# Performance work log

Measured on AMD Instinct MI355X. Metric: run time of the kernel, lower is better.

The kernel has to match this reference:

```python
import jax, jax.numpy as jnp
import numpy as np

NSIDE = 128
NPIX = 12 * NSIDE * NSIDE          # HEALPix pixel count, nested ordering
WIN = 16                           # window = 4x4 nested child block (w=1)
SHIFT = WIN // 2
EPS = 1e-5


def _ln(x, g, b):
    mu = x.mean(-1, keepdims=True)
    var = ((x - mu) ** 2).mean(-1, keepdims=True)
    return (x - mu) * jax.lax.rsqrt(var + EPS) * g + b


def _window_attn(x, wq, bq, wp, bp, n_heads):
    B, N, C = x.shape
    D = C // n_heads
    nw = N // WIN
    qkv = (x @ wq + bq).reshape(B, nw, WIN, 3, n_heads, D)
    q, k, v = jnp.moveaxis(qkv, 3, 0)
    q = jnp.swapaxes(q, 2, 3)
    k = jnp.swapaxes(k, 2, 3)
    v = jnp.swapaxes(v, 2, 3)
    scores = jnp.einsum('bwhqd,bwhkd->bwhqk', q, k) * (D ** -0.5)
    attn = jax.nn.softmax(scores, axis=-1)
    out = jnp.einsum('bwhqk,bwhkd->bwhqd', attn, v)
    out = jnp.swapaxes(out, 2, 3).reshape(B, N, C)
    return out @ wp + bp


def _transformer_block(x, p, shift, n_heads):
    if shift:
        x = jnp.roll(x, -SHIFT, axis=1)          # cyclic shift along nested index
    x = x + _window_attn(_ln(x, p['ln1_g'], p['ln1_b']),
                         p['w_qkv'], p['b_qkv'], p['w_proj'], p['b_proj'], n_heads)
    h = _ln(x, p['ln2_g'], p['ln2_b'])
    x = x + jax.nn.gelu(h @ p['w_mlp1'] + p['b_mlp1'], approximate=False) @ p['w_mlp2'] + p['b_mlp2']
    if shift:
        x = jnp.roll(x, SHIFT, axis=1)
    return x


def _forward(x, w_ff1, b_ff1, ln1_g, ln1_b, w_qkv, b_qkv, w_proj, b_proj,
             ln2_g, ln2_b, w_mlp1, b_mlp1, w_mlp2, b_mlp2, w_ff2, b_ff2,
             n_heads=4):
    residual = x
    h = jax.nn.gelu(x @ w_ff1 + b_ff1, approximate=False)
    for i, shift in enumerate((False, True)):
        p = dict(ln1_g=ln1_g[i], ln1_b=ln1_b[i], w_qkv=w_qkv[i], b_qkv=b_qkv[i],
                 w_proj=w_proj[i], b_proj=b_proj[i], ln2_g=ln2_g[i], ln2_b=ln2_b[i],
                 w_mlp1=w_mlp1[i], b_mlp1=b_mlp1[i], w_mlp2=w_mlp2[i], b_mlp2=b_mlp2[i])
        h = _transformer_block(h, p, shift, n_heads)
    return residual + h @ w_ff2 + b_ff2


def setup_inputs() -> dict:
    key = jax.random.key(0)
    ks = jax.random.split(key, 8)
    F, C, M = 64, 128, 512  # node_feat_dim, node_hidden_dim, mlp hidden
    s = 0.02
    return {
        'x': jax.random.normal(ks[0], (1, NPIX, F), jnp.float32),
        'w_ff1': jax.random.normal(ks[1], (F, C), jnp.float32) * s,
        'b_ff1': jnp.zeros((C,), jnp.float32),
        'ln1_g': jnp.ones((2, C), jnp.float32),
        'ln1_b': jnp.zeros((2, C), jnp.float32),
        'w_qkv': jax.random.normal(ks[2], (2, C, 3 * C), jnp.float32) * s,
        'b_qkv': jnp.zeros((2, 3 * C), jnp.float32),
        'w_proj': jax.random.normal(ks[3], (2, C, C), jnp.float32) * s,
        'b_proj': jnp.zeros((2, C), jnp.float32),
        'ln2_g': jnp.ones((2, C), jnp.float32),
        'ln2_b': jnp.zeros((2, C), jnp.float32),
        'w_mlp1': jax.random.normal(ks[4], (2, C, M), jnp.float32) * s,
        'b_mlp1': jnp.zeros((2, M), jnp.float32),
        'w_mlp2': jax.random.normal(ks[5], (2, M, C), jnp.float32) * s,
        'b_mlp2': jnp.zeros((2, C), jnp.float32),
        'w_ff2': jax.random.normal(ks[6], (C, F), jnp.float32) * s,
        'b_ff2': jnp.zeros((F,), jnp.float32),
    }


def reference(x, w_ff1, b_ff1, ln1_g, ln1_b, w_qkv, b_qkv, w_proj, b_proj,
              ln2_g, ln2_b, w_mlp1, b_mlp1, w_mlp2, b_mlp2, w_ff2, b_ff2):
    return _forward(x, w_ff1, b_ff1, ln1_g, ln1_b, w_qkv, b_qkv, w_proj, b_proj,
                    ln2_g, ln2_b, w_mlp1, b_mlp1, w_mlp2, b_mlp2, w_ff2, b_ff2)
```

## Files before the change

kernel.cpp:

```cpp
#include <hip/hip_runtime.h>
#include <hip/hip_bf16.h>
#include <math.h>

#define NPIX 196608
#define SCALE_Q 0.17677669529663687f

typedef __attribute__((ext_vector_type(4))) float f32x4;
typedef __attribute__((ext_vector_type(8))) short short8;
typedef __attribute__((ext_vector_type(4))) short short4v;
typedef __hip_bfloat16 bf16;

__device__ __forceinline__ float gelu_f(float x) {
    float yy = 1.5957691216057308f * (x + 0.044715f * x * x * x);
    float e = __expf(yy);
    return x - x * __builtin_amdgcn_rcpf(e + 1.0f);
}
__device__ __forceinline__ float gelu_fast(float x) {
    float e = __expf(-1.702f * x);
    return x * __builtin_amdgcn_rcpf(1.0f + e);
}

__device__ __forceinline__ short bfbits(float f) {
    bf16 h = __float2bfloat16(f);
    return *reinterpret_cast<short*>(&h);
}

__device__ __forceinline__ short8 ldsA(const bf16* buf, int row, int el) {
    return *reinterpret_cast<const short8*>(buf + row * 128 + (el ^ ((row & 7) << 3)));
}
__device__ __forceinline__ short8 ldsA64(const bf16* buf, int row, int el) {
    return *reinterpret_cast<const short8*>(buf + row * 64 + (el ^ ((row & 7) << 3)));
}
__device__ __forceinline__ short8 gld8(const bf16* p) {
    return *reinterpret_cast<const short8*>(p);
}

__device__ __forceinline__ void bar_lds() {
    asm volatile("s_waitcnt lgkmcnt(0)" ::: "memory");
    __builtin_amdgcn_s_barrier();
}

__global__ __launch_bounds__(256) void k_convert(
    const float* __restrict__ wff1, const float* __restrict__ wqkv,
    const float* __restrict__ wproj, const float* __restrict__ wmlp1,
    const float* __restrict__ wmlp2, const float* __restrict__ wff2,
    bf16* __restrict__ dst)
{
    int gid = blockIdx.x * 256 + threadIdx.x;
    if (gid < 8192) {
        int n = gid >> 6, k = gid & 63;
        dst[gid] = __float2bfloat16(wff1[k * 128 + n]);
    } else if (gid < 106496) {
        int r = gid - 8192; int l = r / 49152; r -= l * 49152;
        int n = r >> 7, k = r & 127;
        dst[gid] = __float2bfloat16(wqkv[l * 49152 + k * 384 + n]);
    } else if (gid < 139264) {
        int r = gid - 106496; int l = r / 16384; r -= l * 16384;
        int n = r >> 7, k = r & 127;
        dst[gid] = __float2bfloat16(wproj[l * 16384 + k * 128 + n]);
    } else if (gid < 270336) {
        int r = gid - 139264; int l = r >> 16; r &= 65535;
        int n = r >> 7, k = r & 127;
        dst[gid] = __float2bfloat16(wmlp1[l * 65536 + k * 512 + n]);
    } else if (gid < 401408) {
        int r = gid - 270336; int l = r >> 16; r &= 65535;
        int n = r >> 9, k = r & 511;
        dst[gid] = __float2bfloat16(wmlp2[l * 65536 + k * 128 + n]);
    } else if (gid < 409600) {
        int r = gid - 401408;
        int n = r >> 7, k = r & 127;
        dst[gid] = __float2bfloat16(wff2[k * 64 + n]);
    }
}

template <int OFFSET, int MODE>
__global__ __launch_bounds__(256, 3) void k_block(
    const float* __restrict__ x, float* __restrict__ h,
    const bf16* __restrict__ wf1t, const float* __restrict__ bf1,
    const float* __restrict__ g1, const float* __restrict__ be1,
    const bf16* __restrict__ wqt, const float* __restrict__ bq,
    const bf16* __restrict__ wpt, const float* __restrict__ bp,
    const float* __restrict__ g2, const float* __restrict__ be2,
    const bf16* __restrict__ w1t, const float* __restrict__ b1,
    const bf16* __restrict__ w2t, const float* __restrict__ b2,
    const bf16* __restrict__ wf2t, const float* __restrict__ bf2,
    float* __restrict__ out)
{
    __shared__ __align__(16) bf16 bufA[8192];
    __shared__ __align__(16) bf16 bufB[8192];
    __shared__ __align__(16) bf16 bufC[4096];
    const int tid = threadIdx.x, base = blockIdx.x * 64;
    const int wid = tid >> 6, lrow = tid & 15, lgrp = (tid >> 4) & 3;
    const int cb0 = wid * 32;
    const int hc  = wid * 32;

    f32x4 hraw[2][4];

    if (MODE == 0) {
        short8 wf1[2][2];
#pragma unroll
        for (int nt = 0; nt < 2; ++nt)
#pragma unroll
            for (int kk = 0; kk < 2; ++kk)
                wf1[nt][kk] = gld8(wf1t + (size_t)(cb0 + nt * 16 + lrow) * 64 + kk * 32 + lgrp * 8);
        {
            int row = tid >> 2, q = tid & 3;
#pragma unroll
            for (int s = 0; s < 2; ++s) {
                int gg = q + s * 4;
                const float4* src = reinterpret_cast<const float4*>(x + (size_t)(base + row) * 64 + gg * 8);
                float4 v0 = src[0], v1 = src[1];
                short8 w;
                w[0] = bfbits(v0.x); w[1] = bfbits(v0.y); w[2] = bfbits(v0.z); w[3] = bfbits(v0.w);
                w[4] = bfbits(v1.x); w[5] = bfbits(v1.y); w[6] = bfbits(v1.z); w[7] = bfbits(v1.w);
                *reinterpret_cast<short8*>(&bufC[row * 64 + ((gg * 8) ^ ((row & 7) << 3))]) = w;
            }
        }
        bar_lds();
        short8 xb1[4][2];
#pragma unroll
        for (int tt = 0; tt < 4; ++tt)
#pragma unroll
            for (int kk = 0; kk < 2; ++kk)
                xb1[tt][kk] = ldsA64(bufC, tt * 16 + lrow, kk * 32 + lgrp * 8);
#pragma unroll
        for (int nt = 0; nt < 2; ++nt) {
            float4 bv = *reinterpret_cast<const float4*>(bf1 + cb0 + nt * 16 + lgrp * 4);
#pragma unroll
            for (int tt = 0; tt < 4; ++tt) {
                f32x4 d = {0.f, 0.f, 0.f, 0.f};
#pragma unroll
                for (int kk = 0; kk < 2; ++kk)
                    d = __builtin_amdgcn_mfma_f32_16x16x32_bf16(wf1[nt][kk], xb1[tt][kk], d, 0, 0, 0);
                f32x4 r;
                r[0] = gelu_f(d[0] + bv.x); r[1] = gelu_f(d[1] + bv.y);
                r[2] = gelu_f(d[2] + bv.z); r[3] = gelu_f(d[3] + bv.w);
                hraw[nt][tt] = r;
            }
        }
    } else {
#pragma unroll
        for (int nt = 0; nt < 2; ++nt)
#pragma unroll
            for (int tt = 0; tt < 4; ++tt) {
                int tok = base + OFFSET + tt * 16 + lrow; if (tok >= NPIX) tok -= NPIX;
                float4 hv = *reinterpret_cast<const float4*>(h + (size_t)tok * 128 + cb0 + nt * 16 + lgrp * 4);
                f32x4 r; r[0] = hv.x; r[1] = hv.y; r[2] = hv.z; r[3] = hv.w;
                hraw[nt][tt] = r;
            }
    }

    float2* ws1 = reinterpret_cast<float2*>(bufB);
#pragma unroll
    for (int tt = 0; tt < 4; ++tt) {
        float s = 0.f, q = 0.f;
#pragma unroll
        for (int nt = 0; nt < 2; ++nt)
#pragma unroll
            for (int i = 0; i < 4; ++i) { float v = hraw[nt][tt][i]; s += v; q += v * v; }
        s += __shfl_xor(s, 16, 64); s += __shfl_xor(s, 32, 64);
        q += __shfl_xor(q, 16, 64); q += __shfl_xor(q, 32, 64);
        if (lgrp == 0) { float2 t2; t2.x = s; t2.y = q; ws1[wid * 64 + tt * 16 + lrow] = t2; }
    }
    bar_lds();
    {
        float mu[4], rstd[4];
#pragma unroll
        for (int tt = 0; tt < 4; ++tt) {
            float s = 0.f, q = 0.f;
#pragma unroll
            for (int w = 0; w < 4; ++w) {
                float2 t2 = ws1[w * 64 + tt * 16 + lrow];
                s += t2.x; q += t2.y;
            }
            float m = s * (1.f / 128.f);
            mu[tt] = m;
            rstd[tt] = rsqrtf(q * (1.f / 128.f) - m * m + 1e-5f);
        }
        float4 gv[2], bev[2];
#pragma unroll
        for (int nt = 0; nt < 2; ++nt) {
            gv[nt]  = *reinterpret_cast<const float4*>(g1 + cb0 + nt * 16 + lgrp * 4);
            bev[nt] = *reinterpret_cast<const float4*>(be1 + cb0 + nt * 16 + lgrp * 4);
        }
#pragma unroll
        for (int nt = 0; nt < 2; ++nt)
#pragma unroll
            for (int tt = 0; tt < 4; ++tt) {
                short4v pk;
                pk[0] = bfbits((hraw[nt][tt][0] - mu[tt]) * rstd[tt] * gv[nt].x + bev[nt].x);
                pk[1] = bfbits((hraw[nt][tt][1] - mu[tt]) * rstd[tt] * gv[nt].y + bev[nt].y);
                pk[2] = bfbits((hraw[nt][tt][2] - mu[tt]) * rstd[tt] * gv[nt].z + bev[nt].z);
                pk[3] = bfbits((hraw[nt][tt][3] - mu[tt]) * rstd[tt] * gv[nt].w + bev[nt].w);
                int row = tt * 16 + lrow;
                int c = cb0 + nt * 16 + lgrp * 4;
                *reinterpret_cast<short4v*>(&bufA[row * 128 + (c ^ ((row & 7) << 3))]) = pk;
            }
    }
    short8 wfp[2][4];
#pragma unroll
    for (int nt = 0; nt < 2; ++nt)
#pragma unroll
        for (int kk = 0; kk < 4; ++kk)
            wfp[nt][kk] = gld8(wpt + (size_t)(cb0 + nt * 16 + lrow) * 128 + kk * 32 + lgrp * 8);
    bar_lds();

    short8 xb[4][4];
#pragma unroll
    for (int tt = 0; tt < 4; ++tt)
#pragma unroll
        for (int kk = 0; kk < 4; ++kk)
            xb[tt][kk] = ldsA(bufA, tt * 16 + lrow, kk * 32 + lgrp * 8);
    bar_lds();

#pragma unroll
    for (int qt = 0; qt < 2; ++qt) {
        const int cb = hc + qt * 16;
        float4 bqv = *reinterpret_cast<const float4*>(bq + cb + lgrp * 4);
        short8 wf[4];
#pragma unroll
        for (int kk = 0; kk < 4; ++kk)
            wf[kk] = gld8(wqt + (size_t)(cb + lrow) * 128 + kk * 32 + lgrp * 8);
#pragma unroll
        for (int tt = 0; tt < 4; ++tt) {
            f32x4 d = {0.f, 0.f, 0.f, 0.f};
#pragma unroll
            for (int kk = 0; kk < 4; ++kk)
                d = __builtin_amdgcn_mfma_f32_16x16x32_bf16(wf[kk], xb[tt][kk], d, 0, 0, 0);
            int row = tt * 16 + lrow;
            int c = cb + lgrp * 4;
            short4v pk;
            pk[0] = bfbits((d[0] + bqv.x) * SCALE_Q); pk[1] = bfbits((d[1] + bqv.y) * SCALE_Q);
            pk[2] = bfbits((d[2] + bqv.z) * SCALE_Q); pk[3] = bfbits((d[3] + bqv.w) * SCALE_Q);
            *reinterpret_cast<short4v*>(&bufA[row * 128 + (c ^ ((row & 7) << 3))]) = pk;
        }
    }
#pragma unroll
    for (int kt = 0; kt < 2; ++kt) {
        const int cb = hc + kt * 16;
        float4 bqv = *reinterpret_cast<const float4*>(bq + 128 + cb + lgrp * 4);
        short8 wf[4];
#pragma unroll
        for (int kk = 0; kk < 4; ++kk)
            wf[kk] = gld8(wqt + (size_t)(128 + cb + lrow) * 128 + kk * 32 + lgrp * 8);
#pragma unroll
        for (int tt = 0; tt < 4; ++tt) {
            f32x4 d = {0.f, 0.f, 0.f, 0.f};
#pragma unroll
            for (int kk = 0; kk < 4; ++kk)
                d = __builtin_amdgcn_mfma_f32_16x16x32_bf16(wf[kk], xb[tt][kk], d, 0, 0, 0);
            int row = tt * 16 + lrow;
            int c = cb + lgrp * 4;
            short4v pk;
            pk[0] = bfbits(d[0] + bqv.x); pk[1] = bfbits(d[1] + bqv.y);
            pk[2] = bfbits(d[2] + bqv.z); pk[3] = bfbits(d[3] + bqv.w);
            *reinterpret_cast<short4v*>(&bufB[row * 128 + (c ^ ((row & 7) << 3))]) = pk;
        }
    }
    bf16* vt = bufC + wid * 1024;
#pragma unroll
    for (int half = 0; half < 2; ++half) {
#pragma unroll
        for (int vt_ = 0; vt_ < 2; ++vt_) {
            const int cb = hc + vt_ * 16;
            float4 bqv = *reinterpret_cast<const float4*>(bq + 256 + cb + lgrp * 4);
            short8 wf[4];
#pragma unroll
            for (int kk = 0; kk < 4; ++kk)
                wf[kk] = gld8(wqt + (size_t)(256 + cb + lrow) * 128 + kk * 32 + lgrp * 8);
#pragma unroll
            for (int t2 = 0; t2 < 2; ++t2) {
                const int tt = half * 2 + t2;
                f32x4 d = {0.f, 0.f, 0.f, 0.f};
#pragma unroll
                for (int kk = 0; kk < 4; ++kk)
                    d = __builtin_amdgcn_mfma_f32_16x16x32_bf16(wf[kk], xb[tt][kk], d, 0, 0, 0);
#pragma unroll
                for (int i = 0; i < 4; ++i) {
                    int dd = vt_ * 16 + lgrp * 4 + i;
                    vt[dd * 32 + ((t2 * 16 + lrow) ^ ((dd & 3) << 3))] =
                        __float2bfloat16(d[i] + ((const float*)&bqv)[i]);
                }
            }
        }
#pragma unroll
        for (int t2 = 0; t2 < 2; ++t2) {
            const int tt = half * 2 + t2;
            const int row = tt * 16 + lrow;
            const int swr = (lrow & 7) << 3;
            short8 aq = *reinterpret_cast<const short8*>(&bufA[row * 128 + ((hc + lgrp * 8) ^ swr)]);
            short8 bk = *reinterpret_cast<const short8*>(&bufB[row * 128 + ((hc + lgrp * 8) ^ swr)]);
            f32x4 z = {0.f, 0.f, 0.f, 0.f};
            f32x4 s = __builtin_amdgcn_mfma_f32_16x16x32_bf16(bk, aq, z, 0, 0, 0);
            float m_ = fmaxf(fmaxf(s[0], s[1]), fmaxf(s[2], s[3]));
            m_ = fmaxf(m_, __shfl_xor(m_, 16, 64));
            m_ = fmaxf(m_, __shfl_xor(m_, 32, 64));
            float e0 = __expf(s[0] - m_), e1 = __expf(s[1] - m_);
            float e2 = __expf(s[2] - m_), e3 = __expf(s[3] - m_);
            float sum = e0 + e1 + e2 + e3;
            sum += __shfl_xor(sum, 16, 64);
            sum += __shfl_xor(sum, 32, 64);
            float r = __builtin_amdgcn_rcpf(sum);
            short4v pp;
            pp[0] = bfbits(e0 * r); pp[1] = bfbits(e1 * r);
            pp[2] = bfbits(e2 * r); pp[3] = bfbits(e3 * r);
            *reinterpret_cast<short4v*>(&bufA[row * 128 + ((hc + lgrp * 4) ^ swr)]) = pp;

            short8 z8 = {0, 0, 0, 0, 0, 0, 0, 0};
            short8 bp_ = z8;
            if (lgrp < 2)
                bp_ = *reinterpret_cast<const short8*>(&bufA[row * 128 + ((hc + lgrp * 8) ^ swr)]);
#pragma unroll
            for (int dt = 0; dt < 2; ++dt) {
                short8 av = z8;
                if (lgrp < 2)
                    av = *reinterpret_cast<const short8*>(
                        &vt[(dt * 16 + lrow) * 32 + ((t2 * 16 + lgrp * 8) ^ ((lrow & 3) << 3))]);
                f32x4 o = __builtin_amdgcn_mfma_f32_16x16x32_bf16(av, bp_, z, 0, 0, 0);
                short4v pk;
                pk[0] = bfbits(o[0]); pk[1] = bfbits(o[1]); pk[2] = bfbits(o[2]); pk[3] = bfbits(o[3]);
                *reinterpret_cast<short4v*>(&bufA[row * 128 + ((hc + dt * 16 + lgrp * 4) ^ swr)]) = pk;
            }
        }
    }
    bar_lds();

    short8 af[4][4];
#pragma unroll
    for (int tt = 0; tt < 4; ++tt)
#pragma unroll
        for (int kk = 0; kk < 4; ++kk)
            af[tt][kk] = ldsA(bufA, tt * 16 + lrow, kk * 32 + lgrp * 8);
    f32x4 hres[2][4];
#pragma unroll
    for (int nt = 0; nt < 2; ++nt) {
        float4 bpv = *reinterpret_cast<const float4*>(bp + cb0 + nt * 16 + lgrp * 4);
#pragma unroll
        for (int tt = 0; tt < 4; ++tt) {
            f32x4 d = {0.f, 0.f, 0.f, 0.f};
#pragma unroll
            for (int kk = 0; kk < 4; ++kk)
                d = __builtin_amdgcn_mfma_f32_16x16x32_bf16(wfp[nt][kk], af[tt][kk], d, 0, 0, 0);
            f32x4 r = hraw[nt][tt];
            r[0] += bpv.x + d[0]; r[1] += bpv.y + d[1];
            r[2] += bpv.z + d[2]; r[3] += bpv.w + d[3];
            hres[nt][tt] = r;
        }
    }

    float2* ws2 = reinterpret_cast<float2*>(bufC);
#pragma unroll
    for (int tt = 0; tt < 4; ++tt) {
        float s = 0.f, q = 0.f;
#pragma unroll
        for (int nt = 0; nt < 2; ++nt)
#pragma unroll
            for (int i = 0; i < 4; ++i) { float v = hres[nt][tt][i]; s += v; q += v * v; }
        s += __shfl_xor(s, 16, 64); s += __shfl_xor(s, 32, 64);
        q += __shfl_xor(q, 16, 64); q += __shfl_xor(q, 32, 64);
        if (lgrp == 0) { float2 t2; t2.x = s; t2.y = q; ws2[wid * 64 + tt * 16 + lrow] = t2; }
    }
    bar_lds();
    short8 w1f[2][2][4];
    {
        float mu[4], rstd[4];
#pragma unroll
        for (int tt = 0; tt < 4; ++tt) {
            float s = 0.f, q = 0.f;
#pragma unroll
            for (int w = 0; w < 4; ++w) {
                float2 t2 = ws2[w * 64 + tt * 16 + lrow];
                s += t2.x; q += t2.y;
            }
            float m = s * (1.f / 128.f);
            mu[tt] = m;
            rstd[tt] = rsqrtf(q * (1.f / 128.f) - m * m + 1e-5f);
        }
        float4 gv[2], bev[2];
#pragma unroll
        for (int nt = 0; nt < 2; ++nt) {
            gv[nt]  = *reinterpret_cast<const float4*>(g2 + cb0 + nt * 16 + lgrp * 4);
            bev[nt] = *reinterpret_cast<const float4*>(be2 + cb0 + nt * 16 + lgrp * 4);
        }
#pragma unroll
        for (int nt = 0; nt < 2; ++nt)
#pragma unroll
            for (int tt = 0; tt < 4; ++tt) {
                short4v pk;
                pk[0] = bfbits((hres[nt][tt][0] - mu[tt]) * rstd[tt] * gv[nt].x + bev[nt].x);
                pk[1] = bfbits((hres[nt][tt][1] - mu[tt]) * rstd[tt] * gv[nt].y + bev[nt].y);
                pk[2] = bfbits((hres[nt][tt][2] - mu[tt]) * rstd[tt] * gv[nt].z + bev[nt].z);
                pk[3] = bfbits((hres[nt][tt][3] - mu[tt]) * rstd[tt] * gv[nt].w + bev[nt].w);
                int row = tt * 16 + lrow;
                int c = cb0 + nt * 16 + lgrp * 4;
                *reinterpret_cast<short4v*>(&bufB[row * 128 + (c ^ ((row & 7) << 3))]) = pk;
            }
    }
#pragma unroll
    for (int nt = 0; nt < 2; ++nt)
#pragma unroll
        for (int kk = 0; kk < 4; ++kk)
            w1f[0][nt][kk] = gld8(w1t + (size_t)(cb0 + nt * 16 + lrow) * 128 + kk * 32 + lgrp * 8);
    bar_lds();

    f32x4 acc2[2][4];
#pragma unroll
    for (int nt = 0; nt < 2; ++nt)
#pragma unroll
        for (int tt = 0; tt < 4; ++tt) acc2[nt][tt] = (f32x4){0.f, 0.f, 0.f, 0.f};

#pragma unroll
    for (int ch = 0; ch < 4; ++ch) {
        short8 w2f[2][4];
#pragma unroll
        for (int nt = 0; nt < 2; ++nt)
#pragma unroll
            for (int kk = 0; kk < 4; ++kk)
                w2f[nt][kk] = gld8(w2t + (size_t)(cb0 + nt * 16 + lrow) * 512 + ch * 128 + kk * 32 + lgrp * 8);
        float4 b1v[2];
#pragma unroll
        for (int nt = 0; nt < 2; ++nt)
            b1v[nt] = *reinterpret_cast<const float4*>(b1 + ch * 128 + cb0 + nt * 16 + lgrp * 4);
#pragma unroll
        for (int tt = 0; tt < 4; ++tt) {
            short8 xf[4];
#pragma unroll
            for (int kk = 0; kk < 4; ++kk)
                xf[kk] = ldsA(bufB, tt * 16 + lrow, kk * 32 + lgrp * 8);
#pragma unroll
            for (int nt = 0; nt < 2; ++nt) {
                f32x4 d = {0.f, 0.f, 0.f, 0.f};
#pragma unroll
                for (int kk = 0; kk < 4; ++kk)
                    d = __builtin_amdgcn_mfma_f32_16x16x32_bf16(w1f[ch & 1][nt][kk], xf[kk], d, 0, 0, 0);
                short4v pk;
                pk[0] = bfbits(gelu_fast(d[0] + b1v[nt].x)); pk[1] = bfbits(gelu_fast(d[1] + b1v[nt].y));
                pk[2] = bfbits(gelu_fast(d[2] + b1v[nt].z)); pk[3] = bfbits(gelu_fast(d[3] + b1v[nt].w));
                int row = tt * 16 + lrow;
                int c = cb0 + nt * 16 + lgrp * 4;
                *reinterpret_cast<short4v*>(&bufA[row * 128 + (c ^ ((row & 7) << 3))]) = pk;
            }
        }
        if (ch < 3) {
#pragma unroll
            for (int nt = 0; nt < 2; ++nt)
#pragma unroll
                for (int kk = 0; kk < 4; ++kk)
                    w1f[(ch + 1) & 1][nt][kk] =
                        gld8(w1t + (size_t)((ch + 1) * 128 + cb0 + nt * 16 + lrow) * 128 + kk * 32 + lgrp * 8);
        }
        bar_lds();
#pragma unroll
        for (int tt = 0; tt < 4; ++tt) {
            short8 uf[4];
#pragma unroll
            for (int kk = 0; kk < 4; ++kk)
                uf[kk] = ldsA(bufA, tt * 16 + lrow, kk * 32 + lgrp * 8);
#pragma unroll
            for (int nt = 0; nt < 2; ++nt)
#pragma unroll
                for (int kk = 0; kk < 4; ++kk)
                    acc2[nt][tt] = __builtin_amdgcn_mfma_f32_16x16x32_bf16(
                        w2f[nt][kk], uf[kk], acc2[nt][tt], 0, 0, 0);
        }
        if (ch < 3) bar_lds();
    }

    if (MODE == 0) {
#pragma unroll
        for (int nt = 0; nt < 2; ++nt) {
            const int n0 = cb0 + nt * 16 + lgrp * 4;
            float4 b2v = *reinterpret_cast<const float4*>(b2 + n0);
#pragma unroll
            for (int tt = 0; tt < 4; ++tt) {
                int tok = base + OFFSET + tt * 16 + lrow; if (tok >= NPIX) tok -= NPIX;
                float4 ov;
                ov.x = hres[nt][tt][0] + b2v.x + acc2[nt][tt][0];
                ov.y = hres[nt][tt][1] + b2v.y + acc2[nt][tt][1];
                ov.z = hres[nt][tt][2] + b2v.z + acc2[nt][tt][2];
                ov.w = hres[nt][tt][3] + b2v.w + acc2[nt][tt][3];
                *reinterpret_cast<float4*>(h + (size_t)tok * 128 + n0) = ov;
            }
        }
    } else {
        short8 wff[4];
#pragma unroll
        for (int kk = 0; kk < 4; ++kk)
            wff[kk] = gld8(wf2t + (size_t)(wid * 16 + lrow) * 128 + kk * 32 + lgrp * 8);
        float4 xv[4];
#pragma unroll
        for (int tt = 0; tt < 4; ++tt) {
            int tok = base + OFFSET + tt * 16 + lrow; if (tok >= NPIX) tok -= NPIX;
            xv[tt] = *reinterpret_cast<const float4*>(x + (size_t)tok * 64 + wid * 16 + lgrp * 4);
        }
#pragma unroll
        for (int nt = 0; nt < 2; ++nt) {
            const int n0 = cb0 + nt * 16 + lgrp * 4;
            float4 b2v = *reinterpret_cast<const float4*>(b2 + n0);
#pragma unroll
            for (int tt = 0; tt < 4; ++tt) {
                short4v pk;
                pk[0] = bfbits(hres[nt][tt][0] + b2v.x + acc2[nt][tt][0]);
                pk[1] = bfbits(hres[nt][tt][1] + b2v.y + acc2[nt][tt][1]);
                pk[2] = bfbits(hres[nt][tt][2] + b2v.z + acc2[nt][tt][2]);
                pk[3] = bfbits(hres[nt][tt][3] + b2v.w + acc2[nt][tt][3]);
                int row = tt * 16 + lrow;
                int c = cb0 + nt * 16 + lgrp * 4;
                *reinterpret_cast<short4v*>(&bufB[row * 128 + (c ^ ((row & 7) << 3))]) = pk;
            }
        }
        bar_lds();
        float4 bfv = *reinterpret_cast<const float4*>(bf2 + wid * 16 + lgrp * 4);
#pragma unroll
        for (int tt = 0; tt < 4; ++tt) {
            short8 bfr[4];
#pragma unroll
            for (int kk = 0; kk < 4; ++kk)
                bfr[kk] = ldsA(bufB, tt * 16 + lrow, kk * 32 + lgrp * 8);
            f32x4 d = {0.f, 0.f, 0.f, 0.f};
#pragma unroll
            for (int kk = 0; kk < 4; ++kk)
                d = __builtin_amdgcn_mfma_f32_16x16x32_bf16(wff[kk], bfr[kk], d, 0, 0, 0);
            int tok = base + OFFSET + tt * 16 + lrow; if (tok >= NPIX) tok -= NPIX;
            float4 ov;
            ov.x = xv[tt].x + bfv.x + d[0]; ov.y = xv[tt].y + bfv.y + d[1];
            ov.z = xv[tt].z + bfv.z + d[2]; ov.w = xv[tt].w + bfv.w + d[3];
            *reinterpret_cast<float4*>(out + (size_t)tok * 64 + wid * 16 + lgrp * 4) = ov;
        }
    }
}

extern "C" void kernel_launch(void* const* d_in, const int* in_sizes, int n_in,
                              void* d_out, int out_size, void* d_ws, size_t ws_size,
                              hipStream_t stream) {
    (void)in_sizes; (void)n_in; (void)out_size; (void)ws_size;
    const float* x      = (const float*)d_in[0];
    const float* w_ff1  = (const float*)d_in[1];
    const float* b_ff1  = (const float*)d_in[2];
    const float* ln1_g  = (const float*)d_in[3];
    const float* ln1_b  = (const float*)d_in[4];
    const float* w_qkv  = (const float*)d_in[5];
    const float* b_qkv  = (const float*)d_in[6];
    const float* w_proj = (const float*)d_in[7];
    const float* b_proj = (const float*)d_in[8];
    const float* ln2_g  = (const float*)d_in[9];
    const float* ln2_b  = (const float*)d_in[10];
    const float* w_mlp1 = (const float*)d_in[11];
    const float* b_mlp1 = (const float*)d_in[12];
    const float* w_mlp2 = (const float*)d_in[13];
    const float* b_mlp2 = (const float*)d_in[14];
    const float* w_ff2  = (const float*)d_in[15];
    const float* b_ff2  = (const float*)d_in[16];
    float* out = (float*)d_out;

    float* h = (float*)d_ws;
    bf16* wbf = (bf16*)((char*)d_ws + (size_t)NPIX * 128 * 4);
    bf16* ff1t  = wbf;
    bf16* qkvt  = wbf + 8192;
    bf16* projt = wbf + 106496;
    bf16* mlp1t = wbf + 139264;
    bf16* mlp2t = wbf + 270336;
    bf16* ff2t  = wbf + 401408;

    k_convert<<<1600, dim3(256), 0, stream>>>(w_ff1, w_qkv, w_proj, w_mlp1, w_mlp2, w_ff2, wbf);

    const int NB = NPIX / 64;
    k_block<0, 0><<<NB, dim3(256), 0, stream>>>(x, h,
        ff1t, b_ff1,
        ln1_g, ln1_b, qkvt, b_qkv, projt, b_proj,
        ln2_g, ln2_b, mlp1t, b_mlp1, mlp2t, b_mlp2,
        ff2t, b_ff2, out);

    k_block<8, 1><<<NB, dim3(256), 0, stream>>>(x, h,
        ff1t, b_ff1,
        ln1_g + 128, ln1_b + 128, qkvt + 49152, b_qkv + 384, projt + 16384, b_proj + 128,
        ln2_g + 128, ln2_b + 128, mlp1t + 65536, b_mlp1 + 512, mlp2t + 65536, b_mlp2 + 128,
        ff2t, b_ff2, out);
}
```

Baseline: 412.6 us.

## Store intermediate activations in bf16 and coalesce global I/O through LDS

The intermediate hidden buffer between the two block kernels is stored as bf16 instead of fp32, halving its write and read traffic. Writes and reads of the buffer, and the final output, are staged through swizzled shared memory so each thread moves contiguous 16-byte chunks per token row instead of scattered fragments. This adds extra LDS passes and barriers, and rounds the residual stream to bf16 between blocks, which loses some accuracy.

```diff
diff --git a/kernel.cpp b/kernel.cpp
--- a/kernel.cpp
+++ b/kernel.cpp
@@ -23,6 +23,10 @@
 __device__ __forceinline__ short bfbits(float f) {
     bf16 h = __float2bfloat16(f);
     return *reinterpret_cast<short*>(&h);
+}
+__device__ __forceinline__ float b2f(short s) {
+    unsigned int u = ((unsigned int)(unsigned short)s) << 16;
+    union { unsigned int u; float f; } c; c.u = u; return c.f;
 }
 
 __device__ __forceinline__ short8 ldsA(const bf16* buf, int row, int el) {
@@ -75,7 +79,7 @@
 
 template <int OFFSET, int MODE>
 __global__ __launch_bounds__(256, 3) void k_block(
-    const float* __restrict__ x, float* __restrict__ h,
+    const float* __restrict__ x, bf16* __restrict__ h,
     const bf16* __restrict__ wf1t, const float* __restrict__ bf1,
     const float* __restrict__ g1, const float* __restrict__ be1,
     const bf16* __restrict__ wqt, const float* __restrict__ bq,
@@ -140,17 +144,29 @@
         }
     } else {
 #pragma unroll
+        for (int it = 0; it < 4; ++it) {
+            int i = it * 256 + tid;
+            int row = i >> 4, ch = i & 15;
+            int tok = base + OFFSET + row; if (tok >= NPIX) tok -= NPIX;
+            short8 v = *reinterpret_cast<const short8*>(h + (size_t)tok * 128 + ch * 8);
+            *reinterpret_cast<short8*>(&bufB[row * 128 + ((ch * 8) ^ ((row & 7) << 3))]) = v;
+        }
+        bar_lds();
+#pragma unroll
         for (int nt = 0; nt < 2; ++nt)
 #pragma unroll
             for (int tt = 0; tt < 4; ++tt) {
-                int tok = base + OFFSET + tt * 16 + lrow; if (tok >= NPIX) tok -= NPIX;
-                float4 hv = *reinterpret_cast<const float4*>(h + (size_t)tok * 128 + cb0 + nt * 16 + lgrp * 4);
-                f32x4 r; r[0] = hv.x; r[1] = hv.y; r[2] = hv.z; r[3] = hv.w;
+                int row = tt * 16 + lrow;
+                int c = cb0 + nt * 16 + lgrp * 4;
+                short4v pk = *reinterpret_cast<const short4v*>(&bufB[row * 128 + (c ^ ((row & 7) << 3))]);
+                f32x4 r;
+                r[0] = b2f(pk[0]); r[1] = b2f(pk[1]); r[2] = b2f(pk[2]); r[3] = b2f(pk[3]);
                 hraw[nt][tt] = r;
             }
     }
 
-    float2* ws1 = reinterpret_cast<float2*>(bufB);
+    float2* ws1 = (MODE == 0) ? reinterpret_cast<float2*>(bufB)
+                              : reinterpret_cast<float2*>(bufC);
 #pragma unroll
     for (int tt = 0; tt < 4; ++tt) {
         float s = 0.f, q = 0.f;
@@ -473,26 +489,28 @@
             float4 b2v = *reinterpret_cast<const float4*>(b2 + n0);
 #pragma unroll
             for (int tt = 0; tt < 4; ++tt) {
-                int tok = base + OFFSET + tt * 16 + lrow; if (tok >= NPIX) tok -= NPIX;
-                float4 ov;
-                ov.x = hres[nt][tt][0] + b2v.x + acc2[nt][tt][0];
-                ov.y = hres[nt][tt][1] + b2v.y + acc2[nt][tt][1];
-                ov.z = hres[nt][tt][2] + b2v.z + acc2[nt][tt][2];
-                ov.w = hres[nt][tt][3] + b2v.w + acc2[nt][tt][3];
-                *reinterpret_cast<float4*>(h + (size_t)tok * 128 + n0) = ov;
-            }
+                short4v pk;
+                pk[0] = bfbits(hres[nt][tt][0] + b2v.x + acc2[nt][tt][0]);
+                pk[1] = bfbits(hres[nt][tt][1] + b2v.y + acc2[nt][tt][1]);
+                pk[2] = bfbits(hres[nt][tt][2] + b2v.z + acc2[nt][tt][2]);
+                pk[3] = bfbits(hres[nt][tt][3] + b2v.w + acc2[nt][tt][3]);
+                int row = tt * 16 + lrow;
+                *reinterpret_cast<short4v*>(&bufB[row * 128 + (n0 ^ ((row & 7) << 3))]) = pk;
+            }
+        }
+        bar_lds();
+#pragma unroll
+        for (int it = 0; it < 4; ++it) {
+            int i = it * 256 + tid;
+            int row = i >> 4, ch = i & 15;
+            short8 v = *reinterpret_cast<const short8*>(&bufB[row * 128 + ((ch * 8) ^ ((row & 7) << 3))]);
+            *reinterpret_cast<short8*>(h + (size_t)(base + row) * 128 + ch * 8) = v;
         }
     } else {
         short8 wff[4];
 #pragma unroll
         for (int kk = 0; kk < 4; ++kk)
             wff[kk] = gld8(wf2t + (size_t)(wid * 16 + lrow) * 128 + kk * 32 + lgrp * 8);
-        float4 xv[4];
-#pragma unroll
-        for (int tt = 0; tt < 4; ++tt) {
-            int tok = base + OFFSET + tt * 16 + lrow; if (tok >= NPIX) tok -= NPIX;
-            xv[tt] = *reinterpret_cast<const float4*>(x + (size_t)tok * 64 + wid * 16 + lgrp * 4);
-        }
 #pragma unroll
         for (int nt = 0; nt < 2; ++nt) {
             const int n0 = cb0 + nt * 16 + lgrp * 4;
@@ -505,11 +523,12 @@
                 pk[2] = bfbits(hres[nt][tt][2] + b2v.z + acc2[nt][tt][2]);
                 pk[3] = bfbits(hres[nt][tt][3] + b2v.w + acc2[nt][tt][3]);
                 int row = tt * 16 + lrow;
-                int c = cb0 + nt * 16 + lgrp * 4;
+                const int c = n0;
                 *reinterpret_cast<short4v*>(&bufB[row * 128 + (c ^ ((row & 7) << 3))]) = pk;
             }
         }
         bar_lds();
+        float* ob = reinterpret_cast<float*>(bufA);
         float4 bfv = *reinterpret_cast<const float4*>(bf2 + wid * 16 + lgrp * 4);
 #pragma unroll
         for (int tt = 0; tt < 4; ++tt) {
@@ -521,11 +540,25 @@
 #pragma unroll
             for (int kk = 0; kk < 4; ++kk)
                 d = __builtin_amdgcn_mfma_f32_16x16x32_bf16(wff[kk], bfr[kk], d, 0, 0, 0);
-            int tok = base + OFFSET + tt * 16 + lrow; if (tok >= NPIX) tok -= NPIX;
+            int row = tt * 16 + lrow;
+            int c = wid * 16 + lgrp * 4;
+            float4 sv;
+            sv.x = bfv.x + d[0]; sv.y = bfv.y + d[1];
+            sv.z = bfv.z + d[2]; sv.w = bfv.w + d[3];
+            *reinterpret_cast<float4*>(&ob[row * 64 + (c ^ ((row & 7) << 3))]) = sv;
+        }
+        bar_lds();
+#pragma unroll
+        for (int it = 0; it < 4; ++it) {
+            int i = it * 256 + tid;
+            int row = i >> 4, ch = i & 15;
+            int tok = base + OFFSET + row; if (tok >= NPIX) tok -= NPIX;
+            float4 sv = *reinterpret_cast<const float4*>(&ob[row * 64 + ((ch * 4) ^ ((row & 7) << 3))]);
+            float4 xv = *reinterpret_cast<const float4*>(x + (size_t)tok * 64 + ch * 4);
             float4 ov;
-            ov.x = xv[tt].x + bfv.x + d[0]; ov.y = xv[tt].y + bfv.y + d[1];
-            ov.z = xv[tt].z + bfv.z + d[2]; ov.w = xv[tt].w + bfv.w + d[3];
-            *reinterpret_cast<float4*>(out + (size_t)tok * 64 + wid * 16 + lgrp * 4) = ov;
+            ov.x = xv.x + sv.x; ov.y = xv.y + sv.y;
+            ov.z = xv.z + sv.z; ov.w = xv.w + sv.w;
+            *reinterpret_cast<float4*>(out + (size_t)tok * 64 + ch * 4) = ov;
         }
     }
 }
@@ -553,8 +586,8 @@
     const float* b_ff2  = (const float*)d_in[16];
     float* out = (float*)d_out;
 
-    float* h = (float*)d_ws;
-    bf16* wbf = (bf16*)((char*)d_ws + (size_t)NPIX * 128 * 4);
+    bf16* h = (bf16*)d_ws;
+    bf16* wbf = (bf16*)((char*)d_ws + (size_t)NPIX * 128 * 2);
     bf16* ff1t  = wbf;
     bf16* qkvt  = wbf + 8192;
     bf16* projt = wbf + 106496;
```

Result: no change. 414.3 us (+0.4%).
